# Optimization experiments

Hardware: AMD Instinct MI355X
Metric: run time of the kernel (lower is better)

The kernel has to match this reference:

```python
import jax, jax.numpy as jnp
import numpy as np

E = 65536; N = 10000; LAT = 128; K = 8; OH = 128; GD = 64
M0, M1, M2 = 64, 32, 16                 # multiplicities of 0e, 1o, 2e
D_EDGE = M0 + 3 * M1 + 5 * M2           # 240
NG = M1 + M2                            # 48 gate scalars
O0 = M0 + NG                            # 112 scalar outputs of SO2 (scalars + gates)
C0, C1, C2 = 3 * M0, 3 * M1, 3 * M2     # per-l channels of cat(node, edge, node)
FIN0 = C0 + C1 + C2                     # 336 channels at m=0
FIN1 = C1 + C2                          # 144 channels at |m|=1
FIN2 = C2                               # 48 channels at |m|=2
OUT0 = O0 + M1 + M2                     # 160


def _silu(x):
    return x * jax.nn.sigmoid(x)


def _mlp(x, Ws, bs):
    for i, (W, b) in enumerate(zip(Ws, bs)):
        x = x @ W + b
        if i < len(Ws) - 1:
            x = _silu(x)
    return x


def _split(f):
    # [*, 240] -> scalars [*,64], l1 [*,32,3], l2 [*,16,5]
    return (f[:, :M0],
            f[:, M0:M0 + 3 * M1].reshape(-1, M1, 3),
            f[:, M0 + 3 * M1:].reshape(-1, M2, 5))


def forward(latents, node_features, node_onehot, edge_features, edge_vector,
            cutoff_coeffs, edge_one_hot, wigner_D1, wigner_D2, mole_globals,
            Wg, W0, W1r, W1i, W2r, W2i, P0, b0, P1, P2, We, be, ln_g, ln_b,
            M1W0, M1b0, M1W1, M1b1, M1W2, M1b2,
            M2W0, M2b0, M2W1, M2b1, M2W2, M2b2,
            T0, T1, T2, edge_index, active_edges):
    ec = edge_index[0][active_edges]
    en = edge_index[1][active_edges]
    nc = node_features[ec]
    nnb = node_features[en]
    lat_a = latents[active_edges]

    nc0, nc1, nc2 = _split(nc)
    ef0, ef1, ef2 = _split(edge_features)
    nn0, nn1, nn2 = _split(nnb)
    x0 = jnp.concatenate([nc0, ef0, nn0], 1)          # [E,192]
    x1 = jnp.concatenate([nc1, ef1, nn1], 1)          # [E,96,3]
    x2 = jnp.concatenate([nc2, ef2, nn2], 1)          # [E,48,5]

    # rotate into the edge-aligned frame with cached Wigner D matrices
    y1 = jnp.einsum('eij,ecj->eci', wigner_D1, x1)
    y2 = jnp.einsum('eij,ecj->eci', wigner_D2, x2)

    # expert gates: softmax over routed experts + always-on shared expert
    g = jax.nn.softmax(mole_globals @ Wg, axis=-1)    # [E,K]
    gf = jnp.concatenate([g, jnp.ones((g.shape[0], 1), g.dtype)], 1)  # [E,K+1]

    def moe(f, W):  # f [E,F], W [K+1,F,O] -> gated mixture of expert linears
        return jnp.einsum('eko,ek->eo', jnp.einsum('ef,kfo->eko', f, W), gf)

    # SO(2) linear: independent mixing per |m|
    f0 = jnp.concatenate([x0, y1[:, :, 1], y2[:, :, 2]], 1)   # [E,336]
    o0 = moe(f0, W0)                                          # [E,160]
    o0_s, o0_1, o0_2 = o0[:, :O0], o0[:, O0:O0 + M1], o0[:, O0 + M1:]
    fp1 = jnp.concatenate([y1[:, :, 2], y2[:, :, 3]], 1)      # [E,144]
    fm1 = jnp.concatenate([y1[:, :, 0], y2[:, :, 1]], 1)
    op1 = moe(fp1, W1r) - moe(fm1, W1i)                       # [E,48]
    om1 = moe(fp1, W1i) + moe(fm1, W1r)
    fp2, fm2 = y2[:, :, 4], y2[:, :, 0]                       # [E,48]
    op2 = moe(fp2, W2r) - moe(fm2, W2i)                       # [E,16]
    om2 = moe(fp2, W2i) + moe(fm2, W2r)

    z1 = jnp.stack([om1[:, :M1], o0_1, op1[:, :M1]], -1)      # [E,32,3]
    z2 = jnp.stack([om2, om1[:, M1:], o0_2, op1[:, M1:], op2], -1)  # [E,16,5]
    z1 = jnp.einsum('eji,ecj->eci', wigner_D1, z1)            # rotate back (D^T)
    z2 = jnp.einsum('eji,ecj->eci', wigner_D2, z2)

    # Gate activation: silu scalars, sigmoid gates multiply l>0 parts
    sc = _silu(o0_s[:, :M0])
    gates = jax.nn.sigmoid(o0_s[:, M0:])
    v1 = z1 * gates[:, :M1, None]
    v2 = z2 * gates[:, M1:, None]

    # lin_post: per-l channel mixing, bias on scalars only
    sc = sc @ P0 + b0
    v1 = jnp.einsum('ecm,cd->edm', v1, P1)
    v2 = jnp.einsum('ecm,cd->edm', v2, P2)
    scalars = sc                                              # [E,64]

    # E3ElementLinear: per-channel weights generated from latents
    w = lat_a @ We + be                                       # [E,112]
    sc = sc * w[:, :M0]
    v1 = v1 * w[:, M0:M0 + M1, None]
    v2 = v2 * w[:, M0 + M1:, None]
    new_edge = jnp.concatenate([sc, v1.reshape(-1, 3 * M1), v2.reshape(-1, 5 * M2)], 1)

    # latent update: LN -> MLP1(cat scalars) -> MLP2(cat one-hot) -> cutoff
    mu = lat_a.mean(-1, keepdims=True)
    var = ((lat_a - mu) ** 2).mean(-1, keepdims=True)
    ln = (lat_a - mu) * jax.lax.rsqrt(var + 1e-5) * ln_g + ln_b
    nl = _mlp(jnp.concatenate([ln, scalars], 1), [M1W0, M1W1, M1W2], [M1b0, M1b1, M1b2])
    nl = _mlp(jnp.concatenate([nl, edge_one_hot], 1), [M2W0, M2W1, M2W2], [M2b0, M2b1, M2b2])
    nl = cutoff_coeffs[active_edges][:, None] * nl

    # residual update (identity res since irreps_in == irreps_out)
    upd = jax.nn.sigmoid(jnp.zeros((), new_edge.dtype))
    c_old = jax.lax.rsqrt(upd * upd + 1.0)
    c_new = upd * c_old
    edge_out = c_old * edge_features + c_new * new_edge
    latents = latents.at[active_edges].set(c_new * nl + c_old * lat_a)

    # edge one-hot tensor product (uvu, weighted): per-channel scale from one-hot
    s = 1.0 / jnp.sqrt(jnp.asarray(OH, new_edge.dtype))
    t0 = (edge_one_hot @ T0.T) * s                            # [E,64]
    t1 = (edge_one_hot @ T1.T) * s                            # [E,32]
    t2 = (edge_one_hot @ T2.T) * s                            # [E,16]
    e0, e1, e2 = _split(edge_out)
    oh = jnp.concatenate([e0 * t0,
                          (e1 * t1[:, :, None]).reshape(-1, 3 * M1),
                          (e2 * t2[:, :, None]).reshape(-1, 5 * M2)], 1)
    edge_out = edge_out + oh
    return edge_out, latents, wigner_D1, wigner_D2


def setup_inputs():
    key = jax.random.key(0)
    ks = iter(jax.random.split(key, 64))

    def rn(shape, scale=1.0):
        return jax.random.normal(next(ks), shape, dtype=jnp.float32) * scale

    d = {}
    d['latents'] = rn((E, LAT))
    d['node_features'] = rn((N, D_EDGE))
    d['node_onehot'] = rn((N, GD))
    d['edge_features'] = rn((E, D_EDGE))
    ev = rn((E, 3))
    d['edge_vector'] = ev / jnp.linalg.norm(ev, axis=-1, keepdims=True)
    d['cutoff_coeffs'] = jax.random.uniform(next(ks), (E,), dtype=jnp.float32)
    d['edge_one_hot'] = rn((E, OH))
    d['wigner_D1'] = rn((E, 3, 3), 1.0 / np.sqrt(3))
    d['wigner_D2'] = rn((E, 5, 5), 1.0 / np.sqrt(5))
    d['mole_globals'] = rn((E, GD))
    d['edge_index'] = jax.random.randint(next(ks), (2, E), 0, N, dtype=jnp.int32)
    d['active_edges'] = jnp.arange(E, dtype=jnp.int32)
    # parameters
    d['Wg'] = rn((GD, K), 1.0 / np.sqrt(GD))
    d['W0'] = rn((K + 1, FIN0, OUT0), 1.0 / np.sqrt(FIN0))
    d['W1r'] = rn((K + 1, FIN1, NG), 1.0 / np.sqrt(FIN1))
    d['W1i'] = rn((K + 1, FIN1, NG), 1.0 / np.sqrt(FIN1))
    d['W2r'] = rn((K + 1, FIN2, M2), 1.0 / np.sqrt(FIN2))
    d['W2i'] = rn((K + 1, FIN2, M2), 1.0 / np.sqrt(FIN2))
    d['P0'] = rn((M0, M0), 1.0 / np.sqrt(M0)); d['b0'] = jnp.zeros((M0,), jnp.float32)
    d['P1'] = rn((M1, M1), 1.0 / np.sqrt(M1))
    d['P2'] = rn((M2, M2), 1.0 / np.sqrt(M2))
    d['We'] = rn((LAT, M0 + M1 + M2), 1.0 / np.sqrt(LAT))
    d['be'] = jnp.zeros((M0 + M1 + M2,), jnp.float32)
    d['ln_g'] = jnp.ones((LAT,), jnp.float32); d['ln_b'] = jnp.zeros((LAT,), jnp.float32)
    d['M1W0'] = rn((LAT + M0, 128), 1.0 / np.sqrt(LAT + M0)); d['M1b0'] = jnp.zeros((128,), jnp.float32)
    d['M1W1'] = rn((128, 128), 1.0 / np.sqrt(128)); d['M1b1'] = jnp.zeros((128,), jnp.float32)
    d['M1W2'] = rn((128, LAT), 1.0 / np.sqrt(128)); d['M1b2'] = jnp.zeros((LAT,), jnp.float32)
    d['M2W0'] = rn((LAT + OH, 128), 1.0 / np.sqrt(LAT + OH)); d['M2b0'] = jnp.zeros((128,), jnp.float32)
    d['M2W1'] = rn((128, 128), 1.0 / np.sqrt(128)); d['M2b1'] = jnp.zeros((128,), jnp.float32)
    d['M2W2'] = rn((128, LAT), 1.0 / np.sqrt(128)); d['M2b2'] = jnp.zeros((LAT,), jnp.float32)
    d['T0'] = rn((M0, OH), 1.0 / np.sqrt(OH))
    d['T1'] = rn((M1, OH), 1.0 / np.sqrt(OH))
    d['T2'] = rn((M2, OH), 1.0 / np.sqrt(OH))
    return d


def reference(latents, node_features, node_onehot, edge_features, edge_vector,
              cutoff_coeffs, edge_one_hot, wigner_D1, wigner_D2, mole_globals,
              Wg, W0, W1r, W1i, W2r, W2i, P0, b0, P1, P2, We, be, ln_g, ln_b,
              M1W0, M1b0, M1W1, M1b1, M1W2, M1b2,
              M2W0, M2b0, M2W1, M2b1, M2W2, M2b2,
              T0, T1, T2, edge_index, active_edges):
    return forward(latents, node_features, node_onehot, edge_features, edge_vector,
                   cutoff_coeffs, edge_one_hot, wigner_D1, wigner_D2, mole_globals,
                   Wg, W0, W1r, W1i, W2r, W2i, P0, b0, P1, P2, We, be, ln_g, ln_b,
                   M1W0, M1b0, M1W1, M1b1, M1W2, M1b2,
                   M2W0, M2b0, M2W1, M2b1, M2W2, M2b2,
                   T0, T1, T2, edge_index, active_edges)
```

## Files before the change

kernel.cpp:

```cpp
#include <hip/hip_runtime.h>
#include <hip/hip_bf16.h>
#include <stdint.h>

#define EDGES 65536

typedef unsigned int uint;
typedef unsigned short ushort;
using bf16x8 = __attribute__((ext_vector_type(8))) __bf16;
using f32x4  = __attribute__((ext_vector_type(4))) float;
using uintx4 = __attribute__((ext_vector_type(4))) uint;
using float4v = __attribute__((ext_vector_type(4))) float;
using float2v = __attribute__((ext_vector_type(2))) float;

#define C_OLD 0.8944271909999159f
#define C_NEW 0.4472135954999579f
#define T_SCALE 0.08838834764831845f

__device__ __forceinline__ ushort f2bf(float f) {
  uint x = __builtin_bit_cast(uint, f);
  uint r = x + 0x7FFFu + ((x >> 16) & 1u);
  return (ushort)(r >> 16);
}
__device__ __forceinline__ float bf2f(ushort u) {
  uint x = (uint)u << 16;
  return __builtin_bit_cast(float, x);
}
__device__ __forceinline__ void gload16(const void* g, void* l) {
  __builtin_amdgcn_global_load_lds(
      (const __attribute__((address_space(1))) void*)g,
      (__attribute__((address_space(3))) void*)l, 16, 0, 0);
}
template <int N> __device__ __forceinline__ void wait_vm() {
  if constexpr (N <= 0) asm volatile("s_waitcnt vmcnt(0)" ::: "memory");
  else if constexpr (N == 1) asm volatile("s_waitcnt vmcnt(1)" ::: "memory");
  else if constexpr (N == 2) asm volatile("s_waitcnt vmcnt(2)" ::: "memory");
  else if constexpr (N == 3) asm volatile("s_waitcnt vmcnt(3)" ::: "memory");
  else asm volatile("s_waitcnt vmcnt(4)" ::: "memory");
}

struct PackArgs {
  const float *W0, *W1r, *W1i, *W2r, *W2i;
  const float *s0, *s1, *s2, *s3, *s4, *s5, *we, *t0, *t1, *t2, *p0;
  ushort *B0, *B1, *B2;
  ushort *d0, *d1, *d2, *d3, *d4, *d5, *dwe, *dtt, *dp0;
};
#define PACK_BLOCKS 4008
__global__ __launch_bounds__(256) void k_front(
    PackArgs p,
    const float* __restrict__ node_f, const float* __restrict__ edge_f,
    const float* __restrict__ D1g, const float* __restrict__ D2g,
    const float* __restrict__ mg_g, const float* __restrict__ Wg,
    const float* __restrict__ latg, const float* __restrict__ eohg,
    const int* __restrict__ eidx, const int* __restrict__ act,
    ushort* __restrict__ f_all, float* __restrict__ gf_out,
    ushort* __restrict__ lat_bf, ushort* __restrict__ mlp2_in,
    float* __restrict__ out_d1, float* __restrict__ out_d2) {
  __shared__ float sh[4][1244];
  int bid = blockIdx.x;
  if (bid < PACK_BLOCKS) {
    if (bid < 2160) {
      int idx = bid * 256 + threadIdx.x;
      if (idx >= 160 * 3456) return;
      int o = idx / 3456, kf = idx - o * 3456;
      int k = kf / 384, f = kf - k * 384;
      float v = (f < 336) ? p.W0[k * 53760 + f * 160 + o] : 0.f;
      p.B0[idx] = f2bf(v);
    } else if (bid < 3240) {
      int idx = (bid - 2160) * 256 + threadIdx.x;
      if (idx >= 96 * 2880) return;
      int c = idx / 2880, kf = idx - c * 2880;
      int k = kf / 320, f = kf - k * 320;
      float v = 0.f;
      if (f < 288) {
        if (c < 48) v = (f < 144) ? p.W1r[k * 6912 + f * 48 + c] : -p.W1i[k * 6912 + (f - 144) * 48 + c];
        else        v = (f < 144) ? p.W1i[k * 6912 + f * 48 + (c - 48)] : p.W1r[k * 6912 + (f - 144) * 48 + (c - 48)];
      }
      p.B1[idx] = f2bf(v);
    } else if (bid < 3384) {
      int idx = (bid - 3240) * 256 + threadIdx.x;
      if (idx >= 32 * 1152) return;
      int c = idx / 1152, kf = idx - c * 1152;
      int k = kf / 128, f = kf - k * 128;
      float v = 0.f;
      if (f < 96) {
        if (c < 16) v = (f < 48) ? p.W2r[k * 768 + f * 16 + c] : -p.W2i[k * 768 + (f - 48) * 16 + c];
        else        v = (f < 48) ? p.W2i[k * 768 + f * 16 + (c - 16)] : p.W2r[k * 768 + (f - 48) * 16 + (c - 16)];
      }
      p.B2[idx] = f2bf(v);
    } else {
      int idx = (bid - 3384) * 256 + threadIdx.x;
      if (idx < 24576) {
        int n = idx / 192, k = idx - n * 192;
        p.d0[idx] = f2bf(p.s0[k * 128 + n]);
      } else if (idx < 40960) {
        int q = idx - 24576; int n = q >> 7, k = q & 127;
        p.d1[q] = f2bf(p.s1[k * 128 + n]);
      } else if (idx < 57344) {
        int q = idx - 40960; int n = q >> 7, k = q & 127;
        p.d2[q] = f2bf(p.s2[k * 128 + n]);
      } else if (idx < 90112) {
        int q = idx - 57344; int n = q / 256, k = q - n * 256;
        p.d3[q] = f2bf(p.s3[k * 128 + n]);
      } else if (idx < 106496) {
        int q = idx - 90112; int n = q >> 7, k = q & 127;
        p.d4[q] = f2bf(p.s4[k * 128 + n]);
      } else if (idx < 122880) {
        int q = idx - 106496; int n = q >> 7, k = q & 127;
        p.d5[q] = f2bf(p.s5[k * 128 + n]);
      } else if (idx < 139264) {
        int q = idx - 122880; int n = q >> 7, k = q & 127;
        p.dwe[q] = f2bf((n < 112) ? p.we[k * 112 + n] : 0.f);
      } else if (idx < 155648) {
        int q = idx - 139264; int o = q >> 7, h = q & 127;
        float v = 0.f;
        if (o < 64) v = p.t0[o * 128 + h];
        else if (o < 96) v = p.t1[(o - 64) * 128 + h];
        else if (o < 112) v = p.t2[(o - 96) * 128 + h];
        p.dtt[q] = f2bf(v);
      } else if (idx < 159744) {
        int q = idx - 155648; int n = q >> 6, k = q & 63;
        p.dp0[q] = f2bf(p.p0[k * 64 + n]);
      }
    }
    return;
  }
  const int w = threadIdx.x >> 6, lane = threadIdx.x & 63;
  const int e = (bid - PACK_BLOCKS) * 4 + w;
  float* s = sh[w];
  float* s_nc = s;
  float* s_ef = s + 240;
  float* s_nn = s + 480;
  float* s_d1 = s + 720;
  float* s_d2 = s + 729;
  float* s_mg = s + 754;
  float* s_lg = s + 818;
  ushort* row = (ushort*)(s + 828);
  const int ae = act[e];
  const int ec = eidx[ae], en = eidx[EDGES + ae];
  if (lane < 60) {
    ((float4v*)s_nc)[lane] = ((const float4v*)(node_f + (size_t)ec * 240))[lane];
    ((float4v*)s_ef)[lane] = ((const float4v*)(edge_f + (size_t)e * 240))[lane];
    ((float4v*)s_nn)[lane] = ((const float4v*)(node_f + (size_t)en * 240))[lane];
  }
  if (lane < 9)  { float v = D1g[e * 9 + lane];  s_d1[lane] = v; out_d1[(size_t)e * 9 + lane] = v; }
  if (lane < 25) { float v = D2g[e * 25 + lane]; s_d2[lane] = v; out_d2[(size_t)e * 25 + lane] = v; }
  s_mg[lane] = mg_g[e * 64 + lane];
  {
    const float* lp = latg + (size_t)ae * 128;
    float a0 = lp[2 * lane], a1 = lp[2 * lane + 1];
    ((uint*)lat_bf)[(size_t)e * 64 + lane] = (uint)f2bf(a0) | ((uint)f2bf(a1) << 16);
    const float* ep = eohg + (size_t)e * 128;
    a0 = ep[2 * lane]; a1 = ep[2 * lane + 1];
    ((uint*)mlp2_in)[(size_t)e * 128 + 64 + lane] = (uint)f2bf(a0) | ((uint)f2bf(a1) << 16);
  }
  {
    int k = lane & 7, hg = lane >> 3;
    float a = 0.f;
#pragma unroll
    for (int h = 0; h < 8; ++h) a += s_mg[hg * 8 + h] * Wg[(hg * 8 + h) * 8 + k];
    a += __shfl_xor(a, 8);
    a += __shfl_xor(a, 16);
    a += __shfl_xor(a, 32);
    if (lane < 8) s_lg[lane] = a;
  }
  if (lane < 12) {
    float m = s_lg[0];
    for (int j = 1; j < 8; ++j) m = fmaxf(m, s_lg[j]);
    float den = 0.f;
    for (int j = 0; j < 8; ++j) den += __expf(s_lg[j] - m);
    float v = 0.f;
    if (lane < 8) v = __expf(s_lg[lane] - m) / den;
    else if (lane == 8) v = 1.f;
    gf_out[e * 12 + lane] = v;
  }
  row[lane]       = f2bf(s_nc[lane]);
  row[64 + lane]  = f2bf(s_ef[lane]);
  row[128 + lane] = f2bf(s_nn[lane]);
  if (lane < 48) row[336 + lane] = 0;
  if (lane < 32) { row[672 + lane] = 0; row[800 + lane] = 0; }
#pragma unroll
  for (int it = 0; it < 5; ++it) {
    int q = lane + it * 64;
    if (q < 288) {
      int i = q / 96, c = q - i * 96;
      const float* src = (c < 32) ? s_nc : (c < 64) ? s_ef : s_nn;
      int base = 64 + (c & 31) * 3;
      float v = s_d1[i * 3] * src[base] + s_d1[i * 3 + 1] * src[base + 1] + s_d1[i * 3 + 2] * src[base + 2];
      int dst = (i == 0) ? 528 : (i == 1) ? 192 : 384;
      row[dst + c] = f2bf(v);
    }
  }
#pragma unroll
  for (int it = 0; it < 4; ++it) {
    int q = lane + it * 64;
    if (q < 240) {
      int i = q / 48, c = q - i * 48;
      const float* src = (c < 16) ? s_nc : (c < 32) ? s_ef : s_nn;
      int base = 160 + (c & 15) * 5;
      float v = s_d2[i * 5] * src[base] + s_d2[i * 5 + 1] * src[base + 1] +
                s_d2[i * 5 + 2] * src[base + 2] + s_d2[i * 5 + 3] * src[base + 3] +
                s_d2[i * 5 + 4] * src[base + 4];
      int dst = (i == 0) ? 752 : (i == 1) ? 624 : (i == 2) ? 288 : (i == 3) ? 480 : 704;
      row[dst + c] = f2bf(v);
    }
  }
  const uintx4* row4 = (const uintx4*)row;
  uintx4* dst4 = (uintx4*)(f_all + (size_t)e * 832);
#pragma unroll
  for (int it = 0; it < 2; ++it) {
    int q = lane + it * 64;
    if (q < 104) dst4[q] = row4[q];
  }
}

template <int WAVES, int BM, int KZP, int SPG2, int NGRP, int NCOL, int FOFF, int ASTRIDE,
          bool HASBIAS, int EPI>
__device__ __forceinline__ void gemm_dev(
    int bid, char* sm,
    const ushort* __restrict__ A, const ushort* __restrict__ Bt,
    const float* __restrict__ gf, const float* __restrict__ bias,
    ushort* __restrict__ outb, int ob_stride, int ob_off,
    ushort* __restrict__ outb2) {
  constexpr int T = WAVES * 64;
  constexpr int WRS = WAVES / 2;
  constexpr int RPW = BM / WRS;
  constexpr int MI = RPW / 16;
  constexpr int NFW = NCOL / 32;
  constexpr int A_BYTES = BM * 128;
  constexpr int B_BYTES = NCOL * 128;
  constexpr int NT2 = KZP / 64;
  constexpr int AI = (BM * 8) / T;
  constexpr int NB = NCOL * 8;
  constexpr int BI = (NB + T - 1) / T;
  static_assert(NCOL % 32 == 0 && KZP % 64 == 0 && RPW % 16 == 0 && (BM * 8) % T == 0, "geom");
  const int tid = threadIdx.x;
  const int lane = tid & 63, wid = tid >> 6;
  const int wr = wid >> 1, wc = wid & 1;
  const int g16 = lane >> 4;
  const int lane15 = lane & 15;
  const int e0 = bid * BM;
  const f32x4 vzero = {0.f, 0.f, 0.f, 0.f};

  const char* bSrc[BI];
#pragma unroll
  for (int it = 0; it < BI; ++it) {
    int q = tid + it * T;
    if (q < NB) {
      int c = q >> 3, ch = (q & 7) ^ (c & 7);
      bSrc[it] = (const char*)(Bt + (size_t)c * KZP) + ch * 16;
    } else bSrc[it] = nullptr;
  }

  f32x4 accS[MI][NFW];
#pragma unroll
  for (int mi = 0; mi < MI; ++mi)
#pragma unroll
    for (int n = 0; n < NFW; ++n) accS[mi][n] = vzero;

  if constexpr (NGRP > 1) {
    char* b_lds = sm;
    f32x4 accC[MI][NFW];
#pragma unroll
    for (int mi = 0; mi < MI; ++mi)
#pragma unroll
      for (int n = 0; n < NFW; ++n) accC[mi][n] = vzero;

    float gfr[MI][4];
    auto gf_pref = [&](int gx) {
#pragma unroll
      for (int mi = 0; mi < MI; ++mi)
#pragma unroll
        for (int j = 0; j < 4; ++j)
          gfr[mi][j] = gf[(size_t)(e0 + wr * RPW + mi * 16 + g16 * 4 + j) * 12 + gx];
    };
    gf_pref(0);

    bf16x8 afr[SPG2][MI][2];
#pragma unroll
    for (int wi = 0; wi < SPG2; ++wi)
#pragma unroll
      for (int mi = 0; mi < MI; ++mi)
#pragma unroll
        for (int s = 0; s < 2; ++s)
          afr[wi][mi][s] = *(const bf16x8*)(
              A + (size_t)(e0 + wr * RPW + mi * 16 + lane15) * ASTRIDE + FOFF +
              wi * 64 + s * 32 + g16 * 8);

    auto stageB = [&](int t2, int buf) {
#pragma unroll
      for (int it = 0; it < BI; ++it) {
        int q = tid + it * T;
        if (q < NB)
          gload16(bSrc[it] + (size_t)t2 * 128, b_lds + buf * B_BYTES + (tid - lane + it * T) * 16);
      }
    };

    constexpr int FULLI = NB / T;
    constexpr int PARTW = (NB % T) / 64;
    auto wait_tail = [&](bool issued) {
      if (!issued) { wait_vm<0>(); return; }
      if constexpr ((NB % T) == 0) {
        wait_vm<FULLI>();
      } else {
        if (wid < PARTW) wait_vm<FULLI + 1>(); else wait_vm<FULLI>();
      }
    };

    stageB(0, 0);
    stageB(1, 1);
    wait_tail(true);
    __builtin_amdgcn_s_barrier();
    asm volatile("" ::: "memory");

    for (int g = 0; g < NGRP; ++g) {
#pragma unroll
      for (int wi = 0; wi < SPG2; ++wi) {
        int t2 = g * SPG2 + wi;
        bool issue = (t2 + 2) < NT2;
        if (issue) stageB(t2 + 2, (t2 + 2) % 3);
        const char* bL = b_lds + (t2 % 3) * B_BYTES;
#pragma unroll
        for (int s = 0; s < 2; ++s) {
#pragma unroll
          for (int n = 0; n < NFW; ++n) {
            int cB = (wc * NFW + n) * 16 + lane15;
            int slot = (s * 4 + g16) ^ (cB & 7);
            bf16x8 b = *(const bf16x8*)(bL + cB * 128 + slot * 16);
#pragma unroll
            for (int mi = 0; mi < MI; ++mi)
              accC[mi][n] = __builtin_amdgcn_mfma_f32_16x16x32_bf16(afr[wi][mi][s], b, accC[mi][n], 0, 0, 0);
          }
        }
        if (wi == SPG2 - 1) {
#pragma unroll
          for (int mi = 0; mi < MI; ++mi)
#pragma unroll
            for (int n = 0; n < NFW; ++n) {
#pragma unroll
              for (int j = 0; j < 4; ++j) accS[mi][n][j] += gfr[mi][j] * accC[mi][n][j];
              accC[mi][n] = vzero;
            }
          if (g + 1 < NGRP) gf_pref(g + 1);
        }
        wait_tail(issue);
        __builtin_amdgcn_s_barrier();
        asm volatile("" ::: "memory");
      }
    }
  } else {
    char* a_lds = sm;
    char* b_lds = sm + 2 * A_BYTES;
    const char* aSrc[AI];
#pragma unroll
    for (int it = 0; it < AI; ++it) {
      int q = tid + it * T;
      int r = q >> 3, ch = (q & 7) ^ (r & 7);
      aSrc[it] = (const char*)(A + (size_t)(e0 + r) * ASTRIDE + FOFF) + ch * 16;
    }
    auto stage = [&](int t2, int buf) {
#pragma unroll
      for (int it = 0; it < AI; ++it)
        gload16(aSrc[it] + t2 * 128, a_lds + buf * A_BYTES + (tid - lane + it * T) * 16);
#pragma unroll
      for (int it = 0; it < BI; ++it) {
        int q = tid + it * T;
        if (q < NB)
          gload16(bSrc[it] + t2 * 128, b_lds + buf * B_BYTES + (tid - lane + it * T) * 16);
      }
    };
    stage(0, 0);
    __syncthreads();
    int cur = 0;
    for (int t2 = 0; t2 < NT2; ++t2) {
      if (t2 + 1 < NT2) stage(t2 + 1, cur ^ 1);
      const char* aL = a_lds + cur * A_BYTES;
      const char* bL = b_lds + cur * B_BYTES;
#pragma unroll
      for (int s = 0; s < 2; ++s) {
        bf16x8 a[MI];
#pragma unroll
        for (int mi = 0; mi < MI; ++mi) {
          int rA = wr * RPW + mi * 16 + lane15;
          int slot = (s * 4 + g16) ^ (rA & 7);
          a[mi] = *(const bf16x8*)(aL + rA * 128 + slot * 16);
        }
#pragma unroll
        for (int n = 0; n < NFW; ++n) {
          int cB = (wc * NFW + n) * 16 + lane15;
          int slot = (s * 4 + g16) ^ (cB & 7);
          bf16x8 b = *(const bf16x8*)(bL + cB * 128 + slot * 16);
#pragma unroll
          for (int mi = 0; mi < MI; ++mi)
            accS[mi][n] = __builtin_amdgcn_mfma_f32_16x16x32_bf16(a[mi], b, accS[mi][n], 0, 0, 0);
        }
      }
      __syncthreads();
      cur ^= 1;
    }
  }

#pragma unroll
  for (int mi = 0; mi < MI; ++mi) {
    const int row0 = wr * RPW + mi * 16 + g16 * 4;
#pragma unroll
    for (int n = 0; n < NFW; ++n) {
      const int c = (wc * NFW + n) * 16 + lane15;
      float bv = 0.f;
      if constexpr (HASBIAS) bv = bias[c];
#pragma unroll
      for (int j = 0; j < 4; ++j) {
        float v = accS[mi][n][j] + bv;
        const int er = e0 + row0 + j;
        if constexpr (EPI == 1) v = v / (1.f + __expf(-v));
        outb[(size_t)er * ob_stride + ob_off + c] = f2bf(v);
        if constexpr (EPI == 2) {
          if ((wc * NFW + n) * 16 < 64)
            outb2[(size_t)er * 256 + c] = f2bf(v / (1.f + __expf(-v)));
        }
      }
    }
  }
}

struct MoeArgs {
  const ushort *f_all, *B0t, *B1t, *B2t;
  const float* gfb;
  ushort *moeout, *m2in;
};
__global__ __launch_bounds__(512) void k_moe(MoeArgs a) {
  __shared__ char sm[3 * 160 * 128 + 16];
  int bid = blockIdx.x;
  if (bid < 512) {
    gemm_dev<8, 128, 3456, 6, 9, 160, 0, 832, false, 2>(
        bid, sm, a.f_all, a.B0t, a.gfb, nullptr, a.moeout, 288, 0, a.m2in);
  } else if (bid < 1024) {
    gemm_dev<8, 128, 2880, 5, 9, 96, 384, 832, false, 0>(
        bid - 512, sm, a.f_all, a.B1t, a.gfb, nullptr, a.moeout, 288, 160, nullptr);
  } else {
    gemm_dev<8, 128, 1152, 2, 9, 32, 704, 832, false, 0>(
        bid - 1024, sm, a.f_all, a.B2t, a.gfb, nullptr, a.moeout, 288, 256, nullptr);
  }
}

struct Small3Args {
  const ushort *latbf, *Wet, *m2in, *Ttb, *P0t;
  const float* b0;
  ushort *wbuf, *tbuf, *m1in;
};
__global__ __launch_bounds__(256) void k_small3(Small3Args a) {
  __shared__ char sm[49168];
  int bid = blockIdx.x;
  if (bid < 1024) {
    gemm_dev<4, 64, 128, 1, 1, 128, 0, 128, false, 0>(
        bid, sm, a.latbf, a.Wet, nullptr, nullptr, a.wbuf, 128, 0, nullptr);
  } else if (bid < 2048) {
    gemm_dev<4, 64, 128, 1, 1, 128, 128, 256, false, 0>(
        bid - 1024, sm, a.m2in, a.Ttb, nullptr, nullptr, a.tbuf, 128, 0, nullptr);
  } else {
    gemm_dev<4, 64, 64, 1, 1, 64, 0, 256, true, 0>(
        bid - 2048, sm, a.m2in, a.P0t, nullptr, a.b0, a.m1in, 192, 128, nullptr);
  }
}

struct MlpArgs {
  const ushort *m1in, *m2in, *Wt1, *Wt2, *Wt3, *Wt4, *Wt5, *Wt6;
  const float *b1, *b2, *b3, *b4, *b5, *b6;
  const int* act;
  const float *cutg, *latg;
  float* out_lat;
};
__global__ __launch_bounds__(256) void k_mlp(MlpArgs A) {
  __shared__ char sm[61440];
  char* Xa = sm;
  char* Xb = sm + 12288;
  char* Xe = sm + 20480;
  char* W0 = sm + 28672;
  char* W1 = sm + 45056;
  const int tid = threadIdx.x;
  const int lane = tid & 63, w = tid >> 6;
  const int wr = w >> 1, wc = w & 1;
  const int lane15 = lane & 15, g16 = lane >> 4;
  const int e32 = blockIdx.x * 32;
  const f32x4 vzero = {0.f, 0.f, 0.f, 0.f};

  auto stage_w = [&](const ushort* Wt, int K2, int t2, char* dst) {
#pragma unroll
    for (int it = 0; it < 4; ++it) {
      int q = tid + it * 256;
      int c = q >> 3, ch = (q & 7) ^ (c & 7);
      gload16((const char*)Wt + (size_t)c * K2 + t2 * 128 + ch * 16,
              dst + (w + it * 4) * 1024);
    }
  };
  {
#pragma unroll
    for (int it = 0; it < 3; ++it) {
      int q = tid + it * 256;
      int r = q / 24, c24 = q - r * 24;
      int t2 = c24 >> 3, ch = (c24 & 7) ^ (r & 7);
      gload16((const char*)A.m1in + (size_t)(e32 + r) * 384 + t2 * 128 + ch * 16,
              Xa + (w + it * 4) * 1024);
    }
#pragma unroll
    for (int it = 0; it < 2; ++it) {
      int q = tid + it * 256;
      int r = q >> 4, c16 = q & 15;
      int t2 = c16 >> 3, ch = (c16 & 7) ^ (r & 7);
      gload16((const char*)A.m2in + (size_t)(e32 + r) * 512 + 256 + t2 * 128 + ch * 16,
              Xe + (w + it * 4) * 1024);
    }
  }
  stage_w(A.Wt1, 384, 0, W0);
  __syncthreads();

  f32x4 acc[4];
#pragma unroll
  for (int n = 0; n < 4; ++n) acc[n] = vzero;

  auto compute = [&](const char* xin, int xstride, int t2loc, const char* wl) {
#pragma unroll
    for (int s = 0; s < 2; ++s) {
      int row = wr * 16 + lane15;
      bf16x8 a = *(const bf16x8*)(xin + row * xstride + t2loc * 128 + (((s * 4 + g16) ^ (row & 7)) << 4));
#pragma unroll
      for (int n = 0; n < 4; ++n) {
        int cB = wc * 64 + n * 16 + lane15;
        bf16x8 b = *(const bf16x8*)(wl + cB * 128 + (((s * 4 + g16) ^ (cB & 7)) << 4));
        acc[n] = __builtin_amdgcn_mfma_f32_16x16x32_bf16(a, b, acc[n], 0, 0, 0);
      }
    }
  };
  auto epi_x = [&](const float* bias, char* xout, int xstride, bool dosilu) {
#pragma unroll
    for (int n = 0; n < 4; ++n) {
      int c = wc * 64 + n * 16 + lane15;
      float bv = bias[c];
      int ch = (n * 16 + lane15) >> 3;
#pragma unroll
      for (int j = 0; j < 4; ++j) {
        int row = wr * 16 + g16 * 4 + j;
        float v = acc[n][j] + bv;
        if (dosilu) v = v / (1.f + __expf(-v));
        *(ushort*)(xout + row * xstride + wc * 128 + ((ch ^ (row & 7)) << 4) + ((lane15 & 7) << 1)) = f2bf(v);
      }
      acc[n] = vzero;
    }
  };

  stage_w(A.Wt1, 384, 1, W1); compute(Xa, 384, 0, W0); __syncthreads();
  stage_w(A.Wt1, 384, 2, W0); compute(Xa, 384, 1, W1); __syncthreads();
  stage_w(A.Wt2, 256, 0, W1); compute(Xa, 384, 2, W0); epi_x(A.b1, Xb, 256, true); __syncthreads();
  stage_w(A.Wt2, 256, 1, W0); compute(Xb, 256, 0, W1); __syncthreads();
  stage_w(A.Wt3, 256, 0, W1); compute(Xb, 256, 1, W0); epi_x(A.b2, Xa, 384, true); __syncthreads();
  stage_w(A.Wt3, 256, 1, W0); compute(Xa, 384, 0, W1); __syncthreads();
  stage_w(A.Wt4, 512, 0, W1); compute(Xa, 384, 1, W0); epi_x(A.b3, Xb, 256, false); __syncthreads();
  stage_w(A.Wt4, 512, 1, W0); compute(Xb, 256, 0, W1); __syncthreads();
  stage_w(A.Wt4, 512, 2, W1); compute(Xb, 256, 1, W0); __syncthreads();
  stage_w(A.Wt4, 512, 3, W0); compute(Xe, 256, 0, W1); __syncthreads();
  stage_w(A.Wt5, 256, 0, W1); compute(Xe, 256, 1, W0); epi_x(A.b4, Xa, 384, true); __syncthreads();
  stage_w(A.Wt5, 256, 1, W0); compute(Xa, 384, 0, W1); __syncthreads();
  stage_w(A.Wt6, 256, 0, W1); compute(Xa, 384, 1, W0); epi_x(A.b5, Xb, 256, true); __syncthreads();
  stage_w(A.Wt6, 256, 1, W0); compute(Xb, 256, 0, W1); __syncthreads();
  compute(Xb, 256, 1, W0);
#pragma unroll
  for (int n = 0; n < 4; ++n) {
    int c = wc * 64 + n * 16 + lane15;
    float bv = A.b6[c];
#pragma unroll
    for (int j = 0; j < 4; ++j) {
      int row = wr * 16 + g16 * 4 + j;
      int er = e32 + row;
      int ae = A.act[er];
      float v = acc[n][j] + bv;
      A.out_lat[(size_t)ae * 128 + c] = C_NEW * A.cutg[ae] * v + C_OLD * A.latg[(size_t)ae * 128 + c];
    }
  }
}

__global__ __launch_bounds__(512) void k_postf(
    const ushort* __restrict__ moeout,
    const float* __restrict__ D1g, const float* __restrict__ D2g,
    const float* __restrict__ latg, const int* __restrict__ act,
    const float* __restrict__ P1, const float* __restrict__ P2,
    const ushort* __restrict__ wbuf, const float* __restrict__ beg,
    const float* __restrict__ lng, const float* __restrict__ lnb,
    const ushort* __restrict__ tbufp, const float* __restrict__ efg,
    ushort* __restrict__ m1in, float* __restrict__ out_edge) {
  __shared__ float SM[1136 + 8 * 920];
  ushort* Btab = (ushort*)SM;
  float* be_s = SM + 768;
  float* lng_s = SM + 880;
  float* lnb_s = SM + 1008;
  const int t = threadIdx.x;
  const int w = t >> 6, lane = t & 63;
  float* Wp = SM + 1136 + w * 920;
  float* o   = Wp;
  float* row = Wp + 224;
  float* sg  = Wp + 464;
  float* d1  = Wp + 512;
  float* d2  = Wp + 524;
  ushort* wvh = (ushort*)(Wp + 552);
  ushort* tvh = (ushort*)(Wp + 608);
  ushort* tile = (ushort*)(Wp + 664);
  const int e = blockIdx.x * 8 + w;
  const int ae = act[e];
  const f32x4 vzero = {0.f, 0.f, 0.f, 0.f};

  float ef[4];
  ef[0] = efg[(size_t)e * 240 + lane];
  ef[1] = efg[(size_t)e * 240 + 64 + lane];
  ef[2] = efg[(size_t)e * 240 + 128 + lane];
  ef[3] = (lane < 48) ? efg[(size_t)e * 240 + 192 + lane] : 0.f;
  float2v ll = ((const float2v*)(latg + (size_t)ae * 128))[lane];

  if (lane < 28) {
    uintx4 raw = *(const uintx4*)(moeout + (size_t)e * 288 + 64 + lane * 8);
    float* dst = o + lane * 8;
#pragma unroll
    for (int j = 0; j < 4; ++j) {
      uint u = raw[j];
      dst[2 * j] = bf2f((ushort)(u & 0xFFFF));
      dst[2 * j + 1] = bf2f((ushort)(u >> 16));
    }
  }
  if (lane < 14) {
    *(uintx4*)((char*)wvh + lane * 16) = *(const uintx4*)(wbuf + (size_t)e * 128 + lane * 8);
    *(uintx4*)((char*)tvh + lane * 16) = *(const uintx4*)(tbufp + (size_t)e * 128 + lane * 8);
  }
  if (lane < 8) {
    uintx4 raw = *(const uintx4*)(m1in + (size_t)e * 192 + 128 + lane * 8);
    float* dst = row + lane * 8;
#pragma unroll
    for (int j = 0; j < 4; ++j) {
      uint u = raw[j];
      dst[2 * j] = bf2f((ushort)(u & 0xFFFF));
      dst[2 * j + 1] = bf2f((ushort)(u >> 16));
    }
  }
  if (lane < 9)  d1[lane] = D1g[(size_t)e * 9 + lane];
  if (lane < 25) d2[lane] = D2g[(size_t)e * 25 + lane];
  if (lane < 48) sg[lane] = 1.f / (1.f + __expf(-o[lane]));

#pragma unroll
  for (int i = 0; i < 3; ++i) {
    int q = t + i * 512;
    int tbl = q >> 9, idx = q & 511;
    int d = idx >> 5, c = idx & 31;
    float v;
    if (tbl == 0) v = P1[c * 32 + d];
    else if (tbl == 1) v = P1[c * 32 + 16 + d];
    else v = (c < 16) ? P2[c * 16 + d] : 0.f;
    Btab[tbl * 512 + d * 32 + (((c >> 3) ^ (d & 3)) << 3) + (c & 7)] = f2bf(v);
  }
  if (t < 368) {
    if (t < 112) be_s[t] = beg[t];
    else if (t < 240) lng_s[t - 112] = lng[t - 112];
    else lnb_s[t - 240] = lnb[t - 240];
  }

  float sum = ll[0] + ll[1];
  float sq = ll[0] * ll[0] + ll[1] * ll[1];
#pragma unroll
  for (int m = 32; m > 0; m >>= 1) {
    sum += __shfl_xor(sum, m);
    sq += __shfl_xor(sq, m);
  }
  const float mu = sum * (1.f / 128.f);
  const float rs = rsqrtf(sq * (1.f / 128.f) - mu * mu + 1e-5f);

  __syncthreads();

  {
    int i = 2 * lane;
    float l0 = (ll[0] - mu) * rs * lng_s[i] + lnb_s[i];
    float l1 = (ll[1] - mu) * rs * lng_s[i + 1] + lnb_s[i + 1];
    ((uint*)m1in)[(size_t)e * 96 + lane] = (uint)f2bf(l0) | ((uint)f2bf(l1) << 16);
  }
#pragma unroll
  for (int rr = 0; rr < 2; ++rr) {
    int r = lane + rr * 64;
    if (r < 96) {
      int m = r >> 5, c = r & 31;
      float v = d1[m] * o[144 + c] + d1[3 + m] * o[48 + c] + d1[6 + m] * o[96 + c];
      tile[m * 32 + (((c >> 3) ^ (m & 3)) << 3) + (c & 7)] = f2bf(v * sg[c]);
    }
  }
#pragma unroll
  for (int rr = 0; rr < 3; ++rr) {
    int r = lane + rr * 64;
    if (r < 160) {
      int rw = 3 + (r >> 5), c = r & 31;
      ushort hv = 0;
      if (c < 16) {
        int m = rw - 3;
        float v = d2[m] * o[208 + c] + d2[5 + m] * o[176 + c] + d2[10 + m] * o[80 + c] +
                  d2[15 + m] * o[128 + c] + d2[20 + m] * o[192 + c];
        hv = f2bf(v * sg[32 + c]);
      }
      tile[rw * 32 + (((c >> 3) ^ (rw & 3)) << 3) + (c & 7)] = hv;
    }
  }
  {
    const int r15 = lane & 15, g = lane >> 4;
    const int fslot = (g ^ (r15 & 3)) << 3;
    bf16x8 afr = *(const bf16x8*)(tile + r15 * 32 + fslot);
    bf16x8 b1a = *(const bf16x8*)(Btab + r15 * 32 + fslot);
    bf16x8 b1b = *(const bf16x8*)(Btab + 512 + r15 * 32 + fslot);
    bf16x8 b2p = *(const bf16x8*)(Btab + 1024 + r15 * 32 + fslot);
    f32x4 v1a = __builtin_amdgcn_mfma_f32_16x16x32_bf16(afr, b1a, vzero, 0, 0, 0);
    f32x4 v1b = __builtin_amdgcn_mfma_f32_16x16x32_bf16(afr, b1b, vzero, 0, 0, 0);
    f32x4 v2r = __builtin_amdgcn_mfma_f32_16x16x32_bf16(afr, b2p, vzero, 0, 0, 0);
    if (g == 0) {
      float s1 = bf2f(wvh[64 + r15]) + be_s[64 + r15];
      row[64 + r15 * 3 + 0] = v1a[0] * s1;
      row[64 + r15 * 3 + 1] = v1a[1] * s1;
      row[64 + r15 * 3 + 2] = v1a[2] * s1;
      float s2 = bf2f(wvh[80 + r15]) + be_s[80 + r15];
      row[64 + (16 + r15) * 3 + 0] = v1b[0] * s2;
      row[64 + (16 + r15) * 3 + 1] = v1b[1] * s2;
      row[64 + (16 + r15) * 3 + 2] = v1b[2] * s2;
      float s3 = bf2f(wvh[96 + r15]) + be_s[96 + r15];
      row[160 + r15 * 5 + 0] = v2r[3] * s3;
    } else if (g == 1) {
      float s3 = bf2f(wvh[96 + r15]) + be_s[96 + r15];
      row[160 + r15 * 5 + 1] = v2r[0] * s3;
      row[160 + r15 * 5 + 2] = v2r[1] * s3;
      row[160 + r15 * 5 + 3] = v2r[2] * s3;
      row[160 + r15 * 5 + 4] = v2r[3] * s3;
    }
  }
  row[lane] = row[lane] * (bf2f(wvh[lane]) + be_s[lane]);
#pragma unroll
  for (int r = 0; r < 4; ++r) {
    int d = lane + r * 64;
    if (r < 3 || lane < 48) {
      float v = C_OLD * ef[r] + C_NEW * row[d];
      int ti = (d < 64) ? d : (d < 160) ? 64 + (d - 64) / 3 : 96 + (d - 160) / 5;
      float f = bf2f(tvh[ti]) * T_SCALE;
      out_edge[(size_t)e * 240 + d] = v * (1.f + f);
    }
  }
}

extern "C" void kernel_launch(void* const* d_in, const int* in_sizes, int n_in,
                              void* d_out, int out_size, void* d_ws, size_t ws_size,
                              hipStream_t stream) {
  const float* latents = (const float*)d_in[0];
  const float* node_f  = (const float*)d_in[1];
  const float* edge_f  = (const float*)d_in[3];
  const float* cutoff  = (const float*)d_in[5];
  const float* eoh     = (const float*)d_in[6];
  const float* D1      = (const float*)d_in[7];
  const float* D2      = (const float*)d_in[8];
  const float* mg      = (const float*)d_in[9];
  const int*   eidx    = (const int*)d_in[10];
  const int*   act     = (const int*)d_in[11];
  const float* Wg      = (const float*)d_in[12];
  const float* W0      = (const float*)d_in[13];
  const float* W1r     = (const float*)d_in[14];
  const float* W1i     = (const float*)d_in[15];
  const float* W2r     = (const float*)d_in[16];
  const float* W2i     = (const float*)d_in[17];
  const float* P0      = (const float*)d_in[18];
  const float* b0      = (const float*)d_in[19];
  const float* P1      = (const float*)d_in[20];
  const float* P2      = (const float*)d_in[21];
  const float* We      = (const float*)d_in[22];
  const float* be      = (const float*)d_in[23];
  const float* lng     = (const float*)d_in[24];
  const float* lnb     = (const float*)d_in[25];
  const float* M1W0_   = (const float*)d_in[26];
  const float* M1b0_   = (const float*)d_in[27];
  const float* M1W1_   = (const float*)d_in[28];
  const float* M1b1_   = (const float*)d_in[29];
  const float* M1W2_   = (const float*)d_in[30];
  const float* M1b2_   = (const float*)d_in[31];
  const float* M2W0_   = (const float*)d_in[32];
  const float* M2b0_   = (const float*)d_in[33];
  const float* M2W1_   = (const float*)d_in[34];
  const float* M2b1_   = (const float*)d_in[35];
  const float* M2W2_   = (const float*)d_in[36];
  const float* M2b2_   = (const float*)d_in[37];
  const float* T0      = (const float*)d_in[38];
  const float* T1      = (const float*)d_in[39];
  const float* T2      = (const float*)d_in[40];

  float* out_edge = (float*)d_out;
  float* out_lat  = out_edge + (size_t)EDGES * 240;
  float* out_d1   = out_lat + (size_t)EDGES * 128;
  float* out_d2   = out_d1 + (size_t)EDGES * 9;

  char* ws = (char*)d_ws;
  size_t off = 0;
  auto alloc = [&](size_t bytes) -> char* {
    char* p = ws + off;
    off += (bytes + 255) & ~size_t(255);
    return p;
  };
  ushort* f_all  = (ushort*)alloc((size_t)EDGES * 832 * 2);
  float*  gfb    = (float*) alloc((size_t)EDGES * 12 * 4);
  ushort* moeout = (ushort*)alloc((size_t)EDGES * 288 * 2);
  ushort* m2in   = (ushort*)alloc((size_t)EDGES * 256 * 2);
  ushort* latbf  = (ushort*)alloc((size_t)EDGES * 128 * 2);
  ushort* wbuf   = (ushort*)alloc((size_t)EDGES * 128 * 2);
  ushort* B0t    = (ushort*)alloc(160 * 3456 * 2);
  ushort* B1t    = (ushort*)alloc(96 * 2880 * 2);
  ushort* B2t    = (ushort*)alloc(32 * 1152 * 2);
  ushort* Wt1    = (ushort*)alloc(128 * 192 * 2);
  ushort* Wt2    = (ushort*)alloc(128 * 128 * 2);
  ushort* Wt3    = (ushort*)alloc(128 * 128 * 2);
  ushort* Wt4    = (ushort*)alloc(128 * 256 * 2);
  ushort* Wt5    = (ushort*)alloc(128 * 128 * 2);
  ushort* Wt6    = (ushort*)alloc(128 * 128 * 2);
  ushort* Wet    = (ushort*)alloc(128 * 128 * 2);
  ushort* Ttb    = (ushort*)alloc(128 * 128 * 2);
  ushort* P0t    = (ushort*)alloc(64 * 64 * 2);

  ushort* m1in = f_all;
  ushort* tbuf = latbf;

  if (ws_size < off) return;

  PackArgs pk = {W0, W1r, W1i, W2r, W2i,
                 M1W0_, M1W1_, M1W2_, M2W0_, M2W1_, M2W2_, We, T0, T1, T2, P0,
                 B0t, B1t, B2t,
                 Wt1, Wt2, Wt3, Wt4, Wt5, Wt6, Wet, Ttb, P0t};
  k_front<<<PACK_BLOCKS + EDGES / 4, 256, 0, stream>>>(
      pk, node_f, edge_f, D1, D2, mg, Wg, latents, eoh, eidx, act,
      f_all, gfb, latbf, m2in, out_d1, out_d2);

  MoeArgs mo = {f_all, B0t, B1t, B2t, gfb, moeout, m2in};
  k_moe<<<1536, 512, 0, stream>>>(mo);

  Small3Args s3 = {latbf, Wet, m2in, Ttb, P0t, b0, wbuf, tbuf, m1in};
  k_small3<<<3072, 256, 0, stream>>>(s3);

  k_postf<<<EDGES / 8, 512, 0, stream>>>(moeout, D1, D2, latents, act, P1, P2,
                                         wbuf, be, lng, lnb, tbuf, edge_f, m1in, out_edge);

  MlpArgs ma = {m1in, m2in, Wt1, Wt2, Wt3, Wt4, Wt5, Wt6,
                M1b0_, M1b1_, M1b2_, M2b0_, M2b1_, M2b2_,
                act, cutoff, latents, out_lat};
  k_mlp<<<EDGES / 32, 256, 0, stream>>>(ma);
}
```

Before: 409.2 us.

## Triple-buffer weight tiles in MLP kernel with vmcnt-based waits

The chained MLP kernel moves from double to triple buffering of weight k-tiles in LDS (a third 16KB buffer, dynamic shared memory raised to 76KB). Loads are issued two stages ahead, and each barrier waits only for the older batch via vmcnt(4) plus lgkmcnt(0), instead of a full __syncthreads drain. The aim is to hide global->LDS weight latency behind MFMA work. The cost is more LDS per block, which may reduce how many blocks fit per CU.

```diff
diff --git a/kernel.cpp b/kernel.cpp
--- a/kernel.cpp
+++ b/kernel.cpp
@@ -36,6 +36,11 @@
   else if constexpr (N == 2) asm volatile("s_waitcnt vmcnt(2)" ::: "memory");
   else if constexpr (N == 3) asm volatile("s_waitcnt vmcnt(3)" ::: "memory");
   else asm volatile("s_waitcnt vmcnt(4)" ::: "memory");
+}
+__device__ __forceinline__ void bar_lgkm() {
+  asm volatile("s_waitcnt lgkmcnt(0)" ::: "memory");
+  __builtin_amdgcn_s_barrier();
+  asm volatile("" ::: "memory");
 }
 
 struct PackArgs {
@@ -470,12 +475,13 @@
   float* out_lat;
 };
 __global__ __launch_bounds__(256) void k_mlp(MlpArgs A) {
-  __shared__ char sm[61440];
+  extern __shared__ char sm[];
   char* Xa = sm;
   char* Xb = sm + 12288;
   char* Xe = sm + 20480;
   char* W0 = sm + 28672;
   char* W1 = sm + 45056;
+  char* W2 = sm + 61440;
   const int tid = threadIdx.x;
   const int lane = tid & 63, w = tid >> 6;
   const int wr = w >> 1, wc = w & 1;
@@ -511,7 +517,8 @@
     }
   }
   stage_w(A.Wt1, 384, 0, W0);
-  __syncthreads();
+  stage_w(A.Wt1, 384, 1, W1);
+  wait_vm<4>(); bar_lgkm();
 
   f32x4 acc[4];
 #pragma unroll
@@ -547,21 +554,21 @@
     }
   };
 
-  stage_w(A.Wt1, 384, 1, W1); compute(Xa, 384, 0, W0); __syncthreads();
-  stage_w(A.Wt1, 384, 2, W0); compute(Xa, 384, 1, W1); __syncthreads();
-  stage_w(A.Wt2, 256, 0, W1); compute(Xa, 384, 2, W0); epi_x(A.b1, Xb, 256, true); __syncthreads();
-  stage_w(A.Wt2, 256, 1, W0); compute(Xb, 256, 0, W1); __syncthreads();
-  stage_w(A.Wt3, 256, 0, W1); compute(Xb, 256, 1, W0); epi_x(A.b2, Xa, 384, true); __syncthreads();
-  stage_w(A.Wt3, 256, 1, W0); compute(Xa, 384, 0, W1); __syncthreads();
-  stage_w(A.Wt4, 512, 0, W1); compute(Xa, 384, 1, W0); epi_x(A.b3, Xb, 256, false); __syncthreads();
-  stage_w(A.Wt4, 512, 1, W0); compute(Xb, 256, 0, W1); __syncthreads();
-  stage_w(A.Wt4, 512, 2, W1); compute(Xb, 256, 1, W0); __syncthreads();
-  stage_w(A.Wt4, 512, 3, W0); compute(Xe, 256, 0, W1); __syncthreads();
-  stage_w(A.Wt5, 256, 0, W1); compute(Xe, 256, 1, W0); epi_x(A.b4, Xa, 384, true); __syncthreads();
-  stage_w(A.Wt5, 256, 1, W0); compute(Xa, 384, 0, W1); __syncthreads();
-  stage_w(A.Wt6, 256, 0, W1); compute(Xa, 384, 1, W0); epi_x(A.b5, Xb, 256, true); __syncthreads();
-  stage_w(A.Wt6, 256, 1, W0); compute(Xb, 256, 0, W1); __syncthreads();
-  compute(Xb, 256, 1, W0);
+  stage_w(A.Wt1, 384, 2, W2); compute(Xa, 384, 0, W0);                              wait_vm<4>(); bar_lgkm();
+  stage_w(A.Wt2, 256, 0, W0); compute(Xa, 384, 1, W1);                              wait_vm<4>(); bar_lgkm();
+  stage_w(A.Wt2, 256, 1, W1); compute(Xa, 384, 2, W2); epi_x(A.b1, Xb, 256, true);  wait_vm<4>(); bar_lgkm();
+  stage_w(A.Wt3, 256, 0, W2); compute(Xb, 256, 0, W0);                              wait_vm<4>(); bar_lgkm();
+  stage_w(A.Wt3, 256, 1, W0); compute(Xb, 256, 1, W1); epi_x(A.b2, Xa, 384, true);  wait_vm<4>(); bar_lgkm();
+  stage_w(A.Wt4, 512, 0, W1); compute(Xa, 384, 0, W2);                              wait_vm<4>(); bar_lgkm();
+  stage_w(A.Wt4, 512, 1, W2); compute(Xa, 384, 1, W0); epi_x(A.b3, Xb, 256, false); wait_vm<4>(); bar_lgkm();
+  stage_w(A.Wt4, 512, 2, W0); compute(Xb, 256, 0, W1);                              wait_vm<4>(); bar_lgkm();
+  stage_w(A.Wt4, 512, 3, W1); compute(Xb, 256, 1, W2);                              wait_vm<4>(); bar_lgkm();
+  stage_w(A.Wt5, 256, 0, W2); compute(Xe, 256, 0, W0);                              wait_vm<4>(); bar_lgkm();
+  stage_w(A.Wt5, 256, 1, W0); compute(Xe, 256, 1, W1); epi_x(A.b4, Xa, 384, true);  wait_vm<4>(); bar_lgkm();
+  stage_w(A.Wt6, 256, 0, W1); compute(Xa, 384, 0, W2);                              wait_vm<4>(); bar_lgkm();
+  stage_w(A.Wt6, 256, 1, W2); compute(Xa, 384, 1, W0); epi_x(A.b5, Xb, 256, true);  wait_vm<4>(); bar_lgkm();
+  compute(Xb, 256, 0, W1);                                                          wait_vm<0>(); bar_lgkm();
+  compute(Xb, 256, 1, W2);
 #pragma unroll
   for (int n = 0; n < 4; ++n) {
     int c = wc * 64 + n * 16 + lane15;
@@ -821,6 +828,13 @@
 
   if (ws_size < off) return;
 
+  static bool mlp_attr_set = false;
+  if (!mlp_attr_set) {
+    hipFuncSetAttribute(reinterpret_cast<const void*>(k_mlp),
+                        hipFuncAttributeMaxDynamicSharedMemorySize, 77824);
+    mlp_attr_set = true;
+  }
+
   PackArgs pk = {W0, W1r, W1i, W2r, W2i,
                  M1W0_, M1W1_, M1W2_, M2W0_, M2W1_, M2W2_, We, T0, T1, T2, P0,
                  B0t, B1t, B2t,
@@ -841,5 +855,5 @@
   MlpArgs ma = {m1in, m2in, Wt1, Wt2, Wt3, Wt4, Wt5, Wt6,
                 M1b0_, M1b1_, M1b2_, M2b0_, M2b1_, M2b2_,
                 act, cutoff, latents, out_lat};
-  k_mlp<<<EDGES / 32, 256, 0, stream>>>(ma);
-}
+  k_mlp<<<EDGES / 32, 256, 77824, stream>>>(ma);
+}
```

Measured after the change: 406.4 us. Within noise of the previous version (-0.7%).
